# Kernel tuning notes

Measured on AMD Instinct MI355X. Metric: run time of the kernel, lower is better.

The kernel has to match this reference:

```python
import jax, jax.numpy as jnp
import numpy as np

DIM = 2048
NUM_HEADS = 16
HEAD_DIM = DIM // NUM_HEADS
ROPE_BASE = 10000.0


def _rotate_half(t):
    t1, t2 = jnp.split(t, 2, axis=-1)
    return jnp.concatenate([-t2, t1], axis=-1)


def _rope_sin_cos(seq_len):
    # fp32 angles, matching RoPE1D
    inv_freq = 1.0 / (ROPE_BASE ** (jnp.arange(0, HEAD_DIM, 2, dtype=jnp.float32) / HEAD_DIM))
    freqs = jnp.arange(seq_len, dtype=jnp.float32)[:, None] * inv_freq[None, :]  # [S, hd/2]
    angles = jnp.concatenate([freqs, freqs], axis=-1)  # [S, hd]
    return jnp.sin(angles), jnp.cos(angles)


def setup_inputs() -> dict:
    key = jax.random.key(0)
    ks = jax.random.split(key, 5)
    B, S = 2, 2048
    x = jax.random.normal(ks[0], (B, S, DIM), dtype=jnp.float32)
    scale = 1.0 / np.sqrt(DIM)
    W_qkv = jax.random.normal(ks[1], (DIM, 3 * DIM), dtype=jnp.float32) * scale
    b_qkv = jnp.zeros((3 * DIM,), dtype=jnp.float32)
    W_proj = jax.random.normal(ks[2], (DIM, DIM), dtype=jnp.float32) * scale
    b_proj = jnp.zeros((DIM,), dtype=jnp.float32)
    return {"x": x, "W_qkv": W_qkv, "b_qkv": b_qkv, "W_proj": W_proj, "b_proj": b_proj}


def reference(x, W_qkv, b_qkv, W_proj, b_proj):
    B, S, D = x.shape
    H, hd = NUM_HEADS, HEAD_DIM
    qkv = x @ W_qkv + b_qkv  # [B, S, 3D]
    qkv = qkv.reshape(B, S, 3, H, hd)
    q, k, v = qkv[:, :, 0], qkv[:, :, 1], qkv[:, :, 2]  # [B, S, H, hd]
    q, k, v = (t.transpose(0, 2, 1, 3) for t in (q, k, v))  # [B, H, S, hd]
    sin, cos = _rope_sin_cos(S)  # [S, hd]
    sin = sin[None, None]
    cos = cos[None, None]
    q = q * cos + _rotate_half(q) * sin
    k = k * cos + _rotate_half(k) * sin
    # scaled dot-product attention (non-causal, no mask, no dropout)
    scale = 1.0 / np.sqrt(hd).astype(np.float32)
    scores = jnp.einsum("bhqd,bhkd->bhqk", q, k) * scale
    attn = jax.nn.softmax(scores, axis=-1)
    out = jnp.einsum("bhqk,bhkd->bhqd", attn, v)  # [B, H, S, hd]
    out = out.transpose(0, 2, 1, 3).reshape(B, S, D)
    return out @ W_proj + b_proj
```

## Files before the change

kernel.cpp:

```cpp
#include <hip/hip_runtime.h>


typedef __attribute__((ext_vector_type(4))) float  f32x4;
typedef __attribute__((ext_vector_type(8))) short  short8;
typedef __attribute__((ext_vector_type(4))) float  fv4;
typedef __attribute__((ext_vector_type(4))) unsigned short us4;

#define MFMA16(accv, av, bv) \
  asm volatile("v_mfma_f32_16x16x32_bf16 %0, %1, %2, %0" : "+v"(accv) : "v"(av), "v"(bv))

__device__ __forceinline__ unsigned short f2bf(float f) {
  unsigned int u = __float_as_uint(f);
  u += 0x7fffu + ((u >> 16) & 1u);
  return (unsigned short)(u >> 16);
}

__device__ __forceinline__ void gl_lds16(const void* g, void* l) {
  __builtin_amdgcn_global_load_lds((const __attribute__((address_space(1))) void*)g,
                                   (__attribute__((address_space(3))) void*)l, 16, 0, 0);
}

__global__ void cvt_f32_bf16(const float* __restrict__ in,
                             unsigned short* __restrict__ out, int n4) {
  int i = blockIdx.x * blockDim.x + threadIdx.x;
  int stride = gridDim.x * blockDim.x;
  for (; i < n4; i += stride) {
    fv4 v = ((const fv4*)in)[i];
    us4 o;
    o[0] = f2bf(v[0]); o[1] = f2bf(v[1]); o[2] = f2bf(v[2]); o[3] = f2bf(v[3]);
    ((us4*)out)[i] = o;
  }
}

__global__ void transpose_cvt(const float* __restrict__ in,
                              unsigned short* __restrict__ out, int R, int C) {
  __shared__ float tile[32][33];
  int c0 = blockIdx.x * 32, r0 = blockIdx.y * 32;
  int tx = threadIdx.x, ty = threadIdx.y;
#pragma unroll
  for (int i = 0; i < 4; i++)
    tile[ty + i * 8][tx] = in[(size_t)(r0 + ty + i * 8) * C + c0 + tx];
  __syncthreads();
#pragma unroll
  for (int i = 0; i < 4; i++)
    out[(size_t)(c0 + ty + i * 8) * R + r0 + tx] = f2bf(tile[tx][ty + i * 8]);
}

__global__ __launch_bounds__(256, 2) void qkv_gemm(
    const unsigned short* __restrict__ A,
    const unsigned short* __restrict__ Bt,
    const float* __restrict__ bias,
    unsigned short* __restrict__ Qo,
    unsigned short* __restrict__ Ko,
    unsigned short* __restrict__ Vo)
{
  __shared__ __align__(16) unsigned short Al[128 * 64];
  __shared__ __align__(16) unsigned short Bl[128 * 64];

  const int NBX = 48, NWG = 1536;
  int bid = blockIdx.x;
  int nid = (bid & 7) * (NWG / 8) + (bid >> 3);
  int by = nid / NBX, bx = nid - by * NBX;

  int tid = threadIdx.x;
  int wv = tid >> 6, lane = tid & 63;
  int wr = wv >> 1, wc = wv & 1;
  int g = lane >> 4, c = lane & 15;

  int m0 = by * 128, n0 = bx * 128;

  f32x4 acc[4][4];
#pragma unroll
  for (int m = 0; m < 4; m++)
#pragma unroll
    for (int n = 0; n < 4; n++)
#pragma unroll
      for (int r = 0; r < 4; r++) acc[m][n][r] = 0.f;

  for (int k0 = 0; k0 < 2048; k0 += 64) {
#pragma unroll
    for (int i = 0; i < 4; i++) {
      int s = wv * 256 + i * 64 + lane;
      int row = s >> 3;
      int cb = (s & 7) ^ (row & 7);
      gl_lds16(A  + (size_t)(m0 + row) * 2048 + k0 + cb * 8,
               Al + (size_t)(wv * 256 + i * 64) * 8);
      gl_lds16(Bt + (size_t)(n0 + row) * 2048 + k0 + cb * 8,
               Bl + (size_t)(wv * 256 + i * 64) * 8);
    }
    __syncthreads();

    short8 af[4][2], bf[4][2];
#pragma unroll
    for (int m = 0; m < 4; m++) {
      int row = wr * 64 + m * 16 + c;
#pragma unroll
      for (int kc = 0; kc < 2; kc++)
        af[m][kc] = *(const short8*)(Al + row * 64 + (((kc * 4 + g) ^ (row & 7)) * 8));
    }
#pragma unroll
    for (int n = 0; n < 4; n++) {
      int gt = 2 * wc + (n & 1) + (n >> 1) * 4;
      int row = gt * 16 + c;
#pragma unroll
      for (int kc = 0; kc < 2; kc++)
        bf[n][kc] = *(const short8*)(Bl + row * 64 + (((kc * 4 + g) ^ (row & 7)) * 8));
    }
#pragma unroll
    for (int m = 0; m < 4; m++)
#pragma unroll
      for (int n = 0; n < 4; n++) {
        MFMA16(acc[m][n], af[m][0], bf[n][0]);
        MFMA16(acc[m][n], af[m][1], bf[n][1]);
      }
    __syncthreads();
  }

  int sel = bx >> 4;
  int h = bx & 15;
  int b = by >> 4;

  int dloc[4];
  float biasv[4];
#pragma unroll
  for (int n = 0; n < 4; n++) {
    int gt = 2 * wc + (n & 1) + (n >> 1) * 4;
    dloc[n] = gt * 16 + c;
    biasv[n] = bias[n0 + dloc[n]];
  }

  if (sel == 2) {
    unsigned short* Vs = Al;
    for (int p = 0; p < 2; p++) {
      if (wr == p) {
#pragma unroll
        for (int m = 0; m < 4; m++)
#pragma unroll
          for (int n = 0; n < 4; n++) {
            int d = dloc[n];
#pragma unroll
            for (int r = 0; r < 4; r++) {
              int srel = m * 16 + 4 * g + r;
              Vs[d * 64 + (srel ^ ((d & 7) << 3))] = f2bf(acc[m][n][r] + biasv[n]);
            }
          }
      }
      __syncthreads();
#pragma unroll
      for (int i = 0; i < 4; i++) {
        int seg = i * 256 + tid;
        int d = seg >> 3, slot = seg & 7;
        short8 val = *(const short8*)(Vs + d * 64 + ((slot ^ (d & 7)) * 8));
        int s_seq = (by & 15) * 128 + p * 64 + slot * 8;
        *(short8*)(Vo + ((size_t)((b * 16 + h) * 128 + d)) * 2048 + s_seq) = val;
      }
      __syncthreads();
    }
  } else {
    unsigned short* outp = (sel == 0) ? Qo : Ko;
    float qscale = (sel == 0) ? 0.08838834764831845f : 1.0f;
    float invf[2];
#pragma unroll
    for (int j = 0; j < 2; j++)
      invf[j] = __expf(-(float)dloc[j] * 0.14391156831212787f);
    int srow_base = (by & 15) * 128 + wr * 64;
#pragma unroll
    for (int m = 0; m < 4; m++) {
#pragma unroll
      for (int j = 0; j < 2; j++) {
        int dlo = dloc[j];
#pragma unroll
        for (int r = 0; r < 4; r++) {
          int s_seq = srow_base + m * 16 + 4 * g + r;
          float ang = (float)s_seq * invf[j];
          float sn, cs;
          __sincosf(ang, &sn, &cs);
          float vlo = acc[m][j][r]     + biasv[j];
          float vhi = acc[m][j + 2][r] + biasv[j + 2];
          float rlo = (vlo * cs - vhi * sn) * qscale;
          float rhi = (vhi * cs + vlo * sn) * qscale;
          size_t base = ((size_t)((b * 16 + h) * 2048 + s_seq)) * 128;
          outp[base + dlo]      = f2bf(rlo);
          outp[base + dlo + 64] = f2bf(rhi);
        }
      }
    }
  }
}

__global__ __launch_bounds__(256, 2) void attn_kernel(
    const unsigned short* __restrict__ Qi,
    const unsigned short* __restrict__ Ki,
    const unsigned short* __restrict__ Vi,
    unsigned short* __restrict__ X2)
{
  __shared__ __align__(16) unsigned short Kl[32 * 128];
  __shared__ __align__(16) unsigned short Vl[128 * 32];
  __shared__ __align__(16) unsigned short Pl[4][16 * 32];

  int bid = blockIdx.x;
  int nid = (bid & 7) * 128 + (bid >> 3);
  int bh = nid >> 5, qt = nid & 31;
  int tid = threadIdx.x, wv = tid >> 6, lane = tid & 63;
  int g = lane >> 4, c = lane & 15;

  int q0 = qt * 64 + wv * 16;
  const unsigned short* Qb = Qi + ((size_t)bh * 2048 + q0) * 128;
  short8 qf[4];
#pragma unroll
  for (int dc = 0; dc < 4; dc++)
    qf[dc] = *(const short8*)(Qb + (size_t)c * 128 + dc * 32 + g * 8);

  f32x4 accO[8];
#pragma unroll
  for (int nt = 0; nt < 8; nt++)
#pragma unroll
    for (int r = 0; r < 4; r++) accO[nt][r] = 0.f;
  float m_run[4], l_run[4];
#pragma unroll
  for (int r = 0; r < 4; r++) { m_run[r] = -3.0e38f; l_run[r] = 0.f; }

  const unsigned short* Kg = Ki + (size_t)bh * 2048 * 128;
  const unsigned short* Vg = Vi + (size_t)bh * 128 * 2048;

  for (int t0 = 0; t0 < 2048; t0 += 32) {
#pragma unroll
    for (int i = 0; i < 2; i++) {
      int s = wv * 128 + i * 64 + lane;
      int trow = s >> 4, cb = (s & 15) ^ (trow & 7);
      gl_lds16(Kg + (size_t)(t0 + trow) * 128 + cb * 8,
               Kl + (size_t)(wv * 128 + i * 64) * 8);
      int d = s >> 2, cb2 = (s & 3) ^ (d & 3);
      gl_lds16(Vg + (size_t)d * 2048 + t0 + cb2 * 8,
               Vl + (size_t)(wv * 128 + i * 64) * 8);
    }
    __syncthreads();

    f32x4 s0, s1;
#pragma unroll
    for (int r = 0; r < 4; r++) { s0[r] = 0.f; s1[r] = 0.f; }
#pragma unroll
    for (int dc = 0; dc < 4; dc++) {
      short8 kf0 = *(const short8*)(Kl + (size_t)c * 128 + (((dc * 4 + g) ^ (c & 7)) * 8));
      short8 kf1 = *(const short8*)(Kl + (size_t)(16 + c) * 128 + (((dc * 4 + g) ^ ((16 + c) & 7)) * 8));
      MFMA16(s0, qf[dc], kf0);
      MFMA16(s1, qf[dc], kf1);
    }

    float p0[4], p1[4], alpha[4];
#pragma unroll
    for (int r = 0; r < 4; r++) {
      float mx = fmaxf(s0[r], s1[r]);
      mx = fmaxf(mx, __shfl_xor(mx, 1));
      mx = fmaxf(mx, __shfl_xor(mx, 2));
      mx = fmaxf(mx, __shfl_xor(mx, 4));
      mx = fmaxf(mx, __shfl_xor(mx, 8));
      float mnew = fmaxf(m_run[r], mx);
      alpha[r] = __expf(m_run[r] - mnew);
      p0[r] = __expf(s0[r] - mnew);
      p1[r] = __expf(s1[r] - mnew);
      float rs = p0[r] + p1[r];
      rs += __shfl_xor(rs, 1); rs += __shfl_xor(rs, 2);
      rs += __shfl_xor(rs, 4); rs += __shfl_xor(rs, 8);
      l_run[r] = l_run[r] * alpha[r] + rs;
      m_run[r] = mnew;
    }
#pragma unroll
    for (int nt = 0; nt < 8; nt++)
#pragma unroll
      for (int r = 0; r < 4; r++) accO[nt][r] *= alpha[r];

    unsigned short* Pw = Pl[wv];
#pragma unroll
    for (int r = 0; r < 4; r++) {
      Pw[(4 * g + r) * 32 + c]      = f2bf(p0[r]);
      Pw[(4 * g + r) * 32 + 16 + c] = f2bf(p1[r]);
    }
    short8 pf = *(const short8*)(Pw + c * 32 + g * 8);
#pragma unroll
    for (int nt = 0; nt < 8; nt++) {
      int d = nt * 16 + c;
      short8 vf = *(const short8*)(Vl + (size_t)d * 32 + ((g ^ (d & 3)) * 8));
      MFMA16(accO[nt], pf, vf);
    }
    __syncthreads();
  }

  float rl[4];
#pragma unroll
  for (int r = 0; r < 4; r++) rl[r] = 1.0f / l_run[r];
  int b = bh >> 4, h = bh & 15;
#pragma unroll
  for (int nt = 0; nt < 8; nt++)
#pragma unroll
    for (int r = 0; r < 4; r++) {
      int qrow = q0 + 4 * g + r;
      X2[((size_t)(b * 2048 + qrow)) * 2048 + h * 128 + nt * 16 + c] =
          f2bf(accO[nt][r] * rl[r]);
    }
}

__global__ __launch_bounds__(256, 2) void proj_gemm(
    const unsigned short* __restrict__ A,
    const unsigned short* __restrict__ Bt,
    const float* __restrict__ bias,
    float* __restrict__ Co)
{
  __shared__ __align__(16) unsigned short Al[128 * 64];
  __shared__ __align__(16) unsigned short Bl[128 * 64];

  const int NBX = 16, NWG = 512;
  int bid = blockIdx.x;
  int nid = (bid & 7) * (NWG / 8) + (bid >> 3);
  int by = nid / NBX, bx = nid - by * NBX;

  int tid = threadIdx.x;
  int wv = tid >> 6, lane = tid & 63;
  int wr = wv >> 1, wc = wv & 1;
  int g = lane >> 4, c = lane & 15;

  int m0 = by * 128, n0 = bx * 128;

  f32x4 acc[4][4];
#pragma unroll
  for (int m = 0; m < 4; m++)
#pragma unroll
    for (int n = 0; n < 4; n++)
#pragma unroll
      for (int r = 0; r < 4; r++) acc[m][n][r] = 0.f;

  for (int k0 = 0; k0 < 2048; k0 += 64) {
#pragma unroll
    for (int i = 0; i < 4; i++) {
      int s = wv * 256 + i * 64 + lane;
      int row = s >> 3;
      int cb = (s & 7) ^ (row & 7);
      gl_lds16(A  + (size_t)(m0 + row) * 2048 + k0 + cb * 8,
               Al + (size_t)(wv * 256 + i * 64) * 8);
      gl_lds16(Bt + (size_t)(n0 + row) * 2048 + k0 + cb * 8,
               Bl + (size_t)(wv * 256 + i * 64) * 8);
    }
    __syncthreads();

    short8 af[4][2], bf[4][2];
#pragma unroll
    for (int m = 0; m < 4; m++) {
      int row = wr * 64 + m * 16 + c;
#pragma unroll
      for (int kc = 0; kc < 2; kc++)
        af[m][kc] = *(const short8*)(Al + row * 64 + (((kc * 4 + g) ^ (row & 7)) * 8));
    }
#pragma unroll
    for (int n = 0; n < 4; n++) {
      int row = wc * 64 + n * 16 + c;
#pragma unroll
      for (int kc = 0; kc < 2; kc++)
        bf[n][kc] = *(const short8*)(Bl + row * 64 + (((kc * 4 + g) ^ (row & 7)) * 8));
    }
#pragma unroll
    for (int m = 0; m < 4; m++)
#pragma unroll
      for (int n = 0; n < 4; n++) {
        MFMA16(acc[m][n], af[m][0], bf[n][0]);
        MFMA16(acc[m][n], af[m][1], bf[n][1]);
      }
    __syncthreads();
  }

#pragma unroll
  for (int m = 0; m < 4; m++)
#pragma unroll
    for (int n = 0; n < 4; n++)
#pragma unroll
      for (int r = 0; r < 4; r++) {
        int row = m0 + wr * 64 + m * 16 + 4 * g + r;
        int col = n0 + wc * 64 + n * 16 + c;
        Co[(size_t)row * 2048 + col] = acc[m][n][r] + bias[col];
      }
}

extern "C" void kernel_launch(void* const* d_in, const int* in_sizes, int n_in,
                              void* d_out, int out_size, void* d_ws, size_t ws_size,
                              hipStream_t stream) {
  (void)in_sizes; (void)n_in; (void)out_size; (void)ws_size;

  const float* x      = (const float*)d_in[0];
  const float* W_qkv  = (const float*)d_in[1];
  const float* b_qkv  = (const float*)d_in[2];
  const float* W_proj = (const float*)d_in[3];
  const float* b_proj = (const float*)d_in[4];
  float* out = (float*)d_out;

  unsigned short* xb     = (unsigned short*)d_ws;
  unsigned short* wqkvT  = xb     + 8388608;
  unsigned short* wprojT = wqkvT  + 12582912;
  unsigned short* Qb     = wprojT + 4194304;
  unsigned short* Kb     = Qb     + 8388608;
  unsigned short* Vtb    = Kb     + 8388608;
  unsigned short* x2     = Vtb    + 8388608;

  cvt_f32_bf16<<<2048, 256, 0, stream>>>(x, xb, 8388608 / 4);
  transpose_cvt<<<dim3(192, 64), dim3(32, 8), 0, stream>>>(W_qkv, wqkvT, 2048, 6144);
  transpose_cvt<<<dim3(64, 64),  dim3(32, 8), 0, stream>>>(W_proj, wprojT, 2048, 2048);
  qkv_gemm<<<1536, 256, 0, stream>>>(xb, wqkvT, b_qkv, Qb, Kb, Vtb);
  attn_kernel<<<1024, 256, 0, stream>>>(Qb, Kb, Vtb, x2);
  proj_gemm<<<512, 256, 0, stream>>>(x2, wprojT, b_proj, out);
}
```

Baseline: 489.5 us.

## Restructure flash attention with larger tiles, double-buffered K/V and exp2 softmax

```diff
diff --git a/kernel.cpp b/kernel.cpp
--- a/kernel.cpp
+++ b/kernel.cpp
@@ -158,7 +158,7 @@
     }
   } else {
     unsigned short* outp = (sel == 0) ? Qo : Ko;
-    float qscale = (sel == 0) ? 0.08838834764831845f : 1.0f;
+    float qscale = (sel == 0) ? (0.08838834764831845f * 1.44269504088896340736f) : 1.0f;
     float invf[2];
 #pragma unroll
     for (int j = 0; j < 2; j++)
@@ -194,109 +194,176 @@
     const unsigned short* __restrict__ Vi,
     unsigned short* __restrict__ X2)
 {
-  __shared__ __align__(16) unsigned short Kl[32 * 128];
-  __shared__ __align__(16) unsigned short Vl[128 * 32];
-  __shared__ __align__(16) unsigned short Pl[4][16 * 32];
+  __shared__ __align__(16) unsigned short Kl[2][64 * 128];
+  __shared__ __align__(16) unsigned short Vl[2][128 * 64];
+  __shared__ __align__(16) unsigned short Pl[4][32 * 64];
 
   int bid = blockIdx.x;
-  int nid = (bid & 7) * 128 + (bid >> 3);
-  int bh = nid >> 5, qt = nid & 31;
+  int nid = (bid & 7) * 64 + (bid >> 3);
+  int bh = nid >> 4, qblk = nid & 15;
   int tid = threadIdx.x, wv = tid >> 6, lane = tid & 63;
   int g = lane >> 4, c = lane & 15;
 
-  int q0 = qt * 64 + wv * 16;
-  const unsigned short* Qb = Qi + ((size_t)bh * 2048 + q0) * 128;
-  short8 qf[4];
-#pragma unroll
-  for (int dc = 0; dc < 4; dc++)
-    qf[dc] = *(const short8*)(Qb + (size_t)c * 128 + dc * 32 + g * 8);
-
-  f32x4 accO[8];
-#pragma unroll
-  for (int nt = 0; nt < 8; nt++)
-#pragma unroll
-    for (int r = 0; r < 4; r++) accO[nt][r] = 0.f;
-  float m_run[4], l_run[4];
-#pragma unroll
-  for (int r = 0; r < 4; r++) { m_run[r] = -3.0e38f; l_run[r] = 0.f; }
-
   const unsigned short* Kg = Ki + (size_t)bh * 2048 * 128;
   const unsigned short* Vg = Vi + (size_t)bh * 128 * 2048;
-
-  for (int t0 = 0; t0 < 2048; t0 += 32) {
-#pragma unroll
-    for (int i = 0; i < 2; i++) {
-      int s = wv * 128 + i * 64 + lane;
-      int trow = s >> 4, cb = (s & 15) ^ (trow & 7);
-      gl_lds16(Kg + (size_t)(t0 + trow) * 128 + cb * 8,
-               Kl + (size_t)(wv * 128 + i * 64) * 8);
-      int d = s >> 2, cb2 = (s & 3) ^ (d & 3);
-      gl_lds16(Vg + (size_t)d * 2048 + t0 + cb2 * 8,
-               Vl + (size_t)(wv * 128 + i * 64) * 8);
-    }
+  const unsigned short* Qb = Qi + ((size_t)bh * 2048 + qblk * 128 + wv * 32) * 128;
+
+  short8 qf[2][4];
+#pragma unroll
+  for (int qt = 0; qt < 2; qt++)
+#pragma unroll
+    for (int dc = 0; dc < 4; dc++)
+      qf[qt][dc] = *(const short8*)(Qb + (size_t)(qt * 16 + c) * 128 + dc * 32 + g * 8);
+
+  f32x4 accO[2][8];
+#pragma unroll
+  for (int qt = 0; qt < 2; qt++)
+#pragma unroll
+    for (int nt = 0; nt < 8; nt++)
+#pragma unroll
+      for (int r = 0; r < 4; r++) accO[qt][nt][r] = 0.f;
+  float m_run[2] = {-3.0e38f, -3.0e38f};
+  float l_run[2] = {0.f, 0.f};
+
+  auto stage = [&](int bsel, int t0) {
+#pragma unroll
+    for (int j = 0; j < 4; j++) {
+      int e = j * 256 + tid;
+      int s = e >> 4, sl = e & 15;
+      gl_lds16(Kg + (size_t)(t0 + s) * 128 + ((sl ^ (s & 7)) * 8),
+               &Kl[bsel][(size_t)(j * 256 + wv * 64) * 8]);
+    }
+#pragma unroll
+    for (int j = 0; j < 4; j++) {
+      int e = j * 256 + tid;
+      int d = e >> 3, sl = e & 7;
+      gl_lds16(Vg + (size_t)d * 2048 + t0 + ((sl ^ (d & 7)) * 8),
+               &Vl[bsel][(size_t)(j * 256 + wv * 64) * 8]);
+    }
+  };
+
+  stage(0, 0);
+  __syncthreads();
+
+  int cur = 0;
+  for (int t = 0; t < 32; t++) {
+    if (t < 31) stage(cur ^ 1, (t + 1) * 64);
+
+    const unsigned short* Kt_ = &Kl[cur][0];
+    const unsigned short* Vt_ = &Vl[cur][0];
+    unsigned short* Pw = &Pl[wv][0];
+
+    f32x4 sc[2][4];
+#pragma unroll
+    for (int qt = 0; qt < 2; qt++)
+#pragma unroll
+      for (int kt = 0; kt < 4; kt++)
+#pragma unroll
+        for (int r = 0; r < 4; r++) sc[qt][kt][r] = 0.f;
+
+#pragma unroll
+    for (int kt = 0; kt < 4; kt++) {
+      short8 kf[4];
+#pragma unroll
+      for (int dc = 0; dc < 4; dc++)
+        kf[dc] = *(const short8*)(Kt_ + (size_t)(kt * 16 + c) * 128 +
+                                  (((dc * 4 + g) ^ (c & 7)) * 8));
+      __builtin_amdgcn_s_setprio(1);
+#pragma unroll
+      for (int dc = 0; dc < 4; dc++) {
+        MFMA16(sc[0][kt], kf[dc], qf[0][dc]);
+        MFMA16(sc[1][kt], kf[dc], qf[1][dc]);
+      }
+      __builtin_amdgcn_s_setprio(0);
+    }
+
+    float mx[2];
+#pragma unroll
+    for (int qt = 0; qt < 2; qt++) {
+      f32x4 mv = sc[qt][0];
+#pragma unroll
+      for (int kt = 1; kt < 4; kt++)
+#pragma unroll
+        for (int r = 0; r < 4; r++) mv[r] = fmaxf(mv[r], sc[qt][kt][r]);
+      float m0 = fmaxf(fmaxf(mv[0], mv[1]), fmaxf(mv[2], mv[3]));
+      m0 = fmaxf(m0, __shfl_xor(m0, 16));
+      m0 = fmaxf(m0, __shfl_xor(m0, 32));
+      mx[qt] = m0;
+    }
+    if (__any((mx[0] > m_run[0]) || (mx[1] > m_run[1]))) {
+#pragma unroll
+      for (int qt = 0; qt < 2; qt++) {
+        float mnew = fmaxf(m_run[qt], mx[qt]);
+        float al = __builtin_exp2f(m_run[qt] - mnew);
+        l_run[qt] *= al;
+        m_run[qt] = mnew;
+#pragma unroll
+        for (int r = 0; r < 4; r++) {
+          float alr = __shfl(al, 4 * g + r);
+#pragma unroll
+          for (int nt = 0; nt < 8; nt++) accO[qt][nt][r] *= alr;
+        }
+      }
+    }
+#pragma unroll
+    for (int qt = 0; qt < 2; qt++) {
+      float rs = 0.f;
+#pragma unroll
+      for (int kt = 0; kt < 4; kt++) {
+        float p0 = __builtin_exp2f(sc[qt][kt][0] - m_run[qt]);
+        float p1 = __builtin_exp2f(sc[qt][kt][1] - m_run[qt]);
+        float p2 = __builtin_exp2f(sc[qt][kt][2] - m_run[qt]);
+        float p3 = __builtin_exp2f(sc[qt][kt][3] - m_run[qt]);
+        rs += (p0 + p1) + (p2 + p3);
+        unsigned int lo, hi;
+        asm("v_cvt_pk_bf16_f32 %0, %1, %2" : "=v"(lo) : "v"(p0), "v"(p1));
+        asm("v_cvt_pk_bf16_f32 %0, %1, %2" : "=v"(hi) : "v"(p2), "v"(p3));
+        uint2 pk; pk.x = lo; pk.y = hi;
+        *(uint2*)(Pw + (size_t)(qt * 16 + c) * 64 +
+                  (((kt * 2 + (g >> 1)) ^ (c & 7)) * 8) + (g & 1) * 4) = pk;
+      }
+      rs += __shfl_xor(rs, 16);
+      rs += __shfl_xor(rs, 32);
+      l_run[qt] += rs;
+    }
+
+    short8 pa[2][2];
+#pragma unroll
+    for (int qt = 0; qt < 2; qt++)
+#pragma unroll
+      for (int kc = 0; kc < 2; kc++)
+        pa[qt][kc] = *(const short8*)(Pw + (size_t)(qt * 16 + c) * 64 +
+                                      (((kc * 4 + g) ^ (c & 7)) * 8));
+#pragma unroll
+    for (int nt = 0; nt < 8; nt++) {
+      short8 vf0 = *(const short8*)(Vt_ + (size_t)(nt * 16 + c) * 64 +
+                                    ((g ^ (c & 7)) * 8));
+      short8 vf1 = *(const short8*)(Vt_ + (size_t)(nt * 16 + c) * 64 +
+                                    (((4 + g) ^ (c & 7)) * 8));
+      __builtin_amdgcn_s_setprio(1);
+      MFMA16(accO[0][nt], pa[0][0], vf0);
+      MFMA16(accO[1][nt], pa[1][0], vf0);
+      MFMA16(accO[0][nt], pa[0][1], vf1);
+      MFMA16(accO[1][nt], pa[1][1], vf1);
+      __builtin_amdgcn_s_setprio(0);
+    }
+
     __syncthreads();
-
-    f32x4 s0, s1;
-#pragma unroll
-    for (int r = 0; r < 4; r++) { s0[r] = 0.f; s1[r] = 0.f; }
-#pragma unroll
-    for (int dc = 0; dc < 4; dc++) {
-      short8 kf0 = *(const short8*)(Kl + (size_t)c * 128 + (((dc * 4 + g) ^ (c & 7)) * 8));
-      short8 kf1 = *(const short8*)(Kl + (size_t)(16 + c) * 128 + (((dc * 4 + g) ^ ((16 + c) & 7)) * 8));
-      MFMA16(s0, qf[dc], kf0);
-      MFMA16(s1, qf[dc], kf1);
-    }
-
-    float p0[4], p1[4], alpha[4];
+    cur ^= 1;
+  }
+
+  float rl[2] = {1.f / l_run[0], 1.f / l_run[1]};
+  int b = bh >> 4, h = bh & 15;
+  size_t rowbase = (size_t)b * 2048 + qblk * 128 + wv * 32;
+#pragma unroll
+  for (int qt = 0; qt < 2; qt++)
 #pragma unroll
     for (int r = 0; r < 4; r++) {
-      float mx = fmaxf(s0[r], s1[r]);
-      mx = fmaxf(mx, __shfl_xor(mx, 1));
-      mx = fmaxf(mx, __shfl_xor(mx, 2));
-      mx = fmaxf(mx, __shfl_xor(mx, 4));
-      mx = fmaxf(mx, __shfl_xor(mx, 8));
-      float mnew = fmaxf(m_run[r], mx);
-      alpha[r] = __expf(m_run[r] - mnew);
-      p0[r] = __expf(s0[r] - mnew);
-      p1[r] = __expf(s1[r] - mnew);
-      float rs = p0[r] + p1[r];
-      rs += __shfl_xor(rs, 1); rs += __shfl_xor(rs, 2);
-      rs += __shfl_xor(rs, 4); rs += __shfl_xor(rs, 8);
-      l_run[r] = l_run[r] * alpha[r] + rs;
-      m_run[r] = mnew;
-    }
-#pragma unroll
-    for (int nt = 0; nt < 8; nt++)
-#pragma unroll
-      for (int r = 0; r < 4; r++) accO[nt][r] *= alpha[r];
-
-    unsigned short* Pw = Pl[wv];
-#pragma unroll
-    for (int r = 0; r < 4; r++) {
-      Pw[(4 * g + r) * 32 + c]      = f2bf(p0[r]);
-      Pw[(4 * g + r) * 32 + 16 + c] = f2bf(p1[r]);
-    }
-    short8 pf = *(const short8*)(Pw + c * 32 + g * 8);
-#pragma unroll
-    for (int nt = 0; nt < 8; nt++) {
-      int d = nt * 16 + c;
-      short8 vf = *(const short8*)(Vl + (size_t)d * 32 + ((g ^ (d & 3)) * 8));
-      MFMA16(accO[nt], pf, vf);
-    }
-    __syncthreads();
-  }
-
-  float rl[4];
-#pragma unroll
-  for (int r = 0; r < 4; r++) rl[r] = 1.0f / l_run[r];
-  int b = bh >> 4, h = bh & 15;
-#pragma unroll
-  for (int nt = 0; nt < 8; nt++)
-#pragma unroll
-    for (int r = 0; r < 4; r++) {
-      int qrow = q0 + 4 * g + r;
-      X2[((size_t)(b * 2048 + qrow)) * 2048 + h * 128 + nt * 16 + c] =
-          f2bf(accO[nt][r] * rl[r]);
+      float rr = __shfl(rl[qt], 4 * g + r);
+      size_t row = rowbase + qt * 16 + 4 * g + r;
+#pragma unroll
+      for (int nt = 0; nt < 8; nt++)
+        X2[row * 2048 + h * 128 + nt * 16 + c] = f2bf(accO[qt][nt][r] * rr);
     }
 }
 
@@ -403,6 +470,6 @@
   transpose_cvt<<<dim3(192, 64), dim3(32, 8), 0, stream>>>(W_qkv, wqkvT, 2048, 6144);
   transpose_cvt<<<dim3(64, 64),  dim3(32, 8), 0, stream>>>(W_proj, wprojT, 2048, 2048);
   qkv_gemm<<<1536, 256, 0, stream>>>(xb, wqkvT, b_qkv, Qb, Kb, Vtb);
-  attn_kernel<<<1024, 256, 0, stream>>>(Qb, Kb, Vtb, x2);
+  attn_kernel<<<512, 256, 0, stream>>>(Qb, Kb, Vtb, x2);
   proj_gemm<<<512, 256, 0, stream>>>(x2, wprojT, b_proj, out);
 }
```

After: 397.6 us. 18.8% less time.
